# Kernel optimization log

Measured on AMD Instinct MI355X. Metric: run time of the kernel, lower is better.

Reference implementation:

```python
import jax, jax.numpy as jnp
import numpy as np

N_NODES = 50000
N_EDGES = 400000


def _gcn_norm(edge_index, num_nodes):
    """Add self-loops and compute symmetric GCN normalization coefficients.

    Returns (src, dst, norm) where out[dst] += norm * h[src].
    """
    loop = jnp.arange(num_nodes, dtype=edge_index.dtype)
    src = jnp.concatenate([edge_index[0], loop])
    dst = jnp.concatenate([edge_index[1], loop])
    ones = jnp.ones(src.shape[0], dtype=jnp.float32)
    deg = jax.ops.segment_sum(ones, dst, num_segments=num_nodes)
    d_inv_sqrt = jnp.where(deg > 0, jax.lax.rsqrt(jnp.maximum(deg, 1.0)), 0.0)
    norm = d_inv_sqrt[src] * d_inv_sqrt[dst]
    return src, dst, norm


def _gcn_conv(x, W, b, src, dst, norm, num_nodes):
    h = x @ W                              # [N, out] dense GEMM first (PyG GCNConv order)
    msg = h[src] * norm[:, None]           # [E+N, out] gather + scale
    agg = jax.ops.segment_sum(msg, dst, num_segments=num_nodes)  # scatter-add
    return agg + b


def setup_inputs() -> dict:
    key = jax.random.key(0)
    k1, k2, k3, k4, k5, k6 = jax.random.split(key, 6)
    x = jax.random.normal(k1, (N_NODES, 128), dtype=jnp.float32)
    edge_index = jax.random.randint(k2, (2, N_EDGES), 0, N_NODES, dtype=jnp.int64)
    # Glorot-ish scaled params
    W1 = jax.random.normal(k3, (128, 512), dtype=jnp.float32) * (1.0 / np.sqrt(128))
    b1 = jnp.zeros((512,), dtype=jnp.float32)
    W2 = jax.random.normal(k4, (512, 250), dtype=jnp.float32) * (1.0 / np.sqrt(512))
    b2 = jnp.zeros((250,), dtype=jnp.float32)
    return {"x": x, "edge_index": edge_index, "W1": W1, "b1": b1, "W2": W2, "b2": b2}


def reference(x, edge_index, W1, b1, W2, b2):
    num_nodes = x.shape[0]
    src, dst, norm = _gcn_norm(edge_index, num_nodes)
    h = _gcn_conv(x, W1, b1, src, dst, norm, num_nodes)
    h = jax.nn.relu(h)
    h = _gcn_conv(h, W2, b2, src, dst, norm, num_nodes)
    return jax.nn.relu(h)
```

## Files before the change

kernel.cpp:

```cpp
#include <hip/hip_runtime.h>

constexpr int NN  = 50000;
constexpr int NE  = 400000;
constexpr int F0  = 128;
constexpr int F1  = 512;
constexpr int F2  = 250;
constexpr int MT64 = 782;
constexpr int SLOT = 64;

typedef short  short8 __attribute__((ext_vector_type(8)));
typedef float  f32x4  __attribute__((ext_vector_type(4)));

__device__ inline unsigned short f2bf(float f) {
    union { float f; unsigned u; } v; v.f = f;
    unsigned u = v.u;
    return (unsigned short)((u + 0x7FFFu + ((u >> 16) & 1u)) >> 16);
}
__device__ inline float bf2f(unsigned short h) {
    union { unsigned u; float f; } v; v.u = ((unsigned)h) << 16;
    return v.f;
}
__device__ inline float bflo(unsigned u) {
    union { unsigned u; float f; } v; v.u = u << 16; return v.f;
}
__device__ inline float bfhi(unsigned u) {
    union { unsigned u; float f; } v; v.u = u & 0xFFFF0000u; return v.f;
}

__global__ void k_build(const int4* __restrict__ src4, const int4* __restrict__ dst4,
                        int* __restrict__ cnt, int* __restrict__ slot) {
    int t = blockIdx.x * 256 + threadIdx.x;
    if (t >= NE / 4) return;
    int4 s = src4[t];
    int4 d = dst4[t];
    int p;
    p = atomicAdd(&cnt[d.x], 1); if (p < SLOT) slot[d.x * SLOT + p] = s.x;
    p = atomicAdd(&cnt[d.y], 1); if (p < SLOT) slot[d.y * SLOT + p] = s.y;
    p = atomicAdd(&cnt[d.z], 1); if (p < SLOT) slot[d.z * SLOT + p] = s.z;
    p = atomicAdd(&cnt[d.w], 1); if (p < SLOT) slot[d.w * SLOT + p] = s.w;
}

__global__ __launch_bounds__(256) void k_prep(
        const float4* __restrict__ x4, const int* __restrict__ cnt,
        ushort4* __restrict__ xs,
        const float* __restrict__ W1, unsigned short* __restrict__ w1t,
        const float* __restrict__ W2, unsigned short* __restrict__ w2t) {
    int b = blockIdx.x;
    if (b < 6250) {
        int t = b * 256 + threadIdx.x;
        float dn = rsqrtf((float)cnt[t >> 5] + 1.0f);
        float4 v = x4[t];
        ushort4 o;
        o.x = f2bf(dn * v.x); o.y = f2bf(dn * v.y);
        o.z = f2bf(dn * v.z); o.w = f2bf(dn * v.w);
        xs[t] = o;
    } else if (b < 6250 + 256) {
        int t = (b - 6250) * 256 + threadIdx.x;
        int n = t >> 7, k = t & 127;
        w1t[t] = f2bf(W1[k * F1 + n]);
    } else {
        int t = (b - 6506) * 256 + threadIdx.x;
        int n = t >> 9, k = t & 511;
        w2t[t] = (n < F2) ? f2bf(W2[k * F2 + n]) : (unsigned short)0;
    }
}

__global__ __launch_bounds__(256) void k_gather1(
        const unsigned int* __restrict__ xs, const int* __restrict__ slot,
        const int* __restrict__ cnt, unsigned int* __restrict__ agg) {
    int n = blockIdx.x * 4 + (threadIdx.x >> 6);
    int c = threadIdx.x & 63;
    if (n >= NN) return;
    int deg = cnt[n]; if (deg > SLOT) deg = SLOT;
    float dn = rsqrtf((float)deg + 1.0f);
    const int* sl = slot + n * SLOT;
    unsigned a = xs[(size_t)n * 64 + c];
    float s0 = bflo(a), s1 = bfhi(a);
    int j = 0;
    for (; j + 8 <= deg; j += 8) {
        int i0 = sl[j],     i1 = sl[j + 1], i2 = sl[j + 2], i3 = sl[j + 3];
        int i4 = sl[j + 4], i5 = sl[j + 5], i6 = sl[j + 6], i7 = sl[j + 7];
        unsigned v0 = xs[(size_t)i0 * 64 + c];
        unsigned v1 = xs[(size_t)i1 * 64 + c];
        unsigned v2 = xs[(size_t)i2 * 64 + c];
        unsigned v3 = xs[(size_t)i3 * 64 + c];
        unsigned v4 = xs[(size_t)i4 * 64 + c];
        unsigned v5 = xs[(size_t)i5 * 64 + c];
        unsigned v6 = xs[(size_t)i6 * 64 + c];
        unsigned v7 = xs[(size_t)i7 * 64 + c];
        s0 += bflo(v0) + bflo(v1) + bflo(v2) + bflo(v3)
            + bflo(v4) + bflo(v5) + bflo(v6) + bflo(v7);
        s1 += bfhi(v0) + bfhi(v1) + bfhi(v2) + bfhi(v3)
            + bfhi(v4) + bfhi(v5) + bfhi(v6) + bfhi(v7);
    }
    for (; j + 4 <= deg; j += 4) {
        int i0 = sl[j], i1 = sl[j + 1], i2 = sl[j + 2], i3 = sl[j + 3];
        unsigned v0 = xs[(size_t)i0 * 64 + c];
        unsigned v1 = xs[(size_t)i1 * 64 + c];
        unsigned v2 = xs[(size_t)i2 * 64 + c];
        unsigned v3 = xs[(size_t)i3 * 64 + c];
        s0 += bflo(v0) + bflo(v1) + bflo(v2) + bflo(v3);
        s1 += bfhi(v0) + bfhi(v1) + bfhi(v2) + bfhi(v3);
    }
    for (; j < deg; ++j) {
        unsigned v = xs[(size_t)sl[j] * 64 + c];
        s0 += bflo(v); s1 += bfhi(v);
    }
    agg[(size_t)n * 64 + c] =
        (unsigned)f2bf(dn * s0) | ((unsigned)f2bf(dn * s1) << 16);
}

__global__ __launch_bounds__(256) void k_gemm1(
        const unsigned short* __restrict__ A,
        const unsigned short* __restrict__ Bt,
        unsigned short* __restrict__ C,
        const float* __restrict__ bias, int M)
{
    __shared__ unsigned short As[64 * 128];
    __shared__ unsigned short Bs[128 * 128];

    const int tid = threadIdx.x;
    const int wv = tid >> 6, ln = tid & 63;
    const int m0 = blockIdx.y * 64, n0 = blockIdx.x * 128;
    const int wy = wv >> 1, wx = wv & 1;
    const int lane15 = ln & 15, quad = ln >> 4;

#pragma unroll
    for (int i = 0; i < 4; ++i) {
        int c = i * 256 + tid;
        int m = c >> 4, q = c & 15;
        int gq = q ^ (m & 15);
        int arow = m0 + m; if (arow > M - 1) arow = M - 1;
        __builtin_amdgcn_global_load_lds(
            (const __attribute__((address_space(1))) void*)(A + (size_t)arow * 128 + gq * 8),
            (__attribute__((address_space(3))) void*)(As + (i * 4 + wv) * 512), 16, 0, 0);
    }
#pragma unroll
    for (int i = 0; i < 8; ++i) {
        int c = i * 256 + tid;
        int n = c >> 4, q = c & 15;
        int gq = q ^ (n & 15);
        __builtin_amdgcn_global_load_lds(
            (const __attribute__((address_space(1))) void*)(Bt + (size_t)(n0 + n) * 128 + gq * 8),
            (__attribute__((address_space(3))) void*)(Bs + (i * 4 + wv) * 512), 16, 0, 0);
    }

    f32x4 acc[2][4];
#pragma unroll
    for (int fy = 0; fy < 2; ++fy)
#pragma unroll
        for (int fx = 0; fx < 4; ++fx)
            acc[fy][fx] = (f32x4)0.0f;

    __syncthreads();

#pragma unroll
    for (int kk = 0; kk < 4; ++kk) {
        short8 af[2], bf[4];
#pragma unroll
        for (int f = 0; f < 2; ++f) {
            int mA = wy * 32 + f * 16 + lane15;
            int sA = (kk * 4 + quad) ^ (mA & 15);
            af[f] = *(const short8*)(As + mA * 128 + sA * 8);
        }
#pragma unroll
        for (int f = 0; f < 4; ++f) {
            int nB = wx * 64 + f * 16 + lane15;
            int sB = (kk * 4 + quad) ^ (nB & 15);
            bf[f] = *(const short8*)(Bs + nB * 128 + sB * 8);
        }
#pragma unroll
        for (int fy = 0; fy < 2; ++fy)
#pragma unroll
            for (int fx = 0; fx < 4; ++fx)
                acc[fy][fx] = __builtin_amdgcn_mfma_f32_16x16x32_bf16(
                    af[fy], bf[fx], acc[fy][fx], 0, 0, 0);
    }

#pragma unroll
    for (int fy = 0; fy < 2; ++fy) {
        int rowb = m0 + wy * 32 + fy * 16 + quad * 4;
#pragma unroll
        for (int fx = 0; fx < 4; ++fx) {
            int col = n0 + wx * 64 + fx * 16 + lane15;
            float bia = bias[col];
            f32x4 v = acc[fy][fx];
#pragma unroll
            for (int r = 0; r < 4; ++r) {
                int row = rowb + r;
                if (row < M)
                    C[(size_t)row * F1 + col] = f2bf(fmaxf(v[r] + bia, 0.0f));
            }
        }
    }
}

__global__ __launch_bounds__(256) void k_gemm2(
        const unsigned short* __restrict__ A,
        const unsigned short* __restrict__ Bt,
        unsigned short* __restrict__ C,
        const int* __restrict__ cnt, int M)
{
    __shared__ unsigned short As[2][64 * 32];
    __shared__ unsigned short Bs[2][256 * 32];

    const int tid = threadIdx.x;
    const int wv = tid >> 6, ln = tid & 63;
    const int m0 = blockIdx.x * 64;
    const int wy = wv >> 1, wx = wv & 1;
    const int lane15 = ln & 15, quad = ln >> 4;

    const int mA_ = tid >> 2, qA = tid & 3;
    const int gqA = qA ^ ((mA_ >> 1) & 3);
    int arow = m0 + mA_; if (arow > M - 1) arow = M - 1;
    const unsigned short* agp = A + (size_t)arow * F1 + gqA * 8;
    const int aofs = wv * 512;

    const unsigned short* bgp[4];
    int bofs[4];
#pragma unroll
    for (int i = 0; i < 4; ++i) {
        int c = (i * 4 + wv) * 64 + ln;
        int n = c >> 2, q = c & 3;
        int gq = q ^ ((n >> 1) & 3);
        bgp[i] = Bt + (size_t)n * F1 + gq * 8;
        bofs[i] = (i * 4 + wv) * 512;
    }

    f32x4 acc[2][8];
#pragma unroll
    for (int fy = 0; fy < 2; ++fy)
#pragma unroll
        for (int fx = 0; fx < 8; ++fx)
            acc[fy][fx] = (f32x4)0.0f;

    const int NK = F1 / 32;

    __builtin_amdgcn_global_load_lds(
        (const __attribute__((address_space(1))) void*)agp,
        (__attribute__((address_space(3))) void*)(&As[0][0] + aofs), 16, 0, 0);
#pragma unroll
    for (int i = 0; i < 4; ++i)
        __builtin_amdgcn_global_load_lds(
            (const __attribute__((address_space(1))) void*)bgp[i],
            (__attribute__((address_space(3))) void*)(&Bs[0][0] + bofs[i]), 16, 0, 0);

    for (int ks = 0; ks < NK; ++ks) {
        __syncthreads();
        if (ks + 1 < NK) {
            int ko = (ks + 1) << 5;
            int nb = (ks + 1) & 1;
            __builtin_amdgcn_global_load_lds(
                (const __attribute__((address_space(1))) void*)(agp + ko),
                (__attribute__((address_space(3))) void*)(&As[nb][0] + aofs), 16, 0, 0);
#pragma unroll
            for (int i = 0; i < 4; ++i)
                __builtin_amdgcn_global_load_lds(
                    (const __attribute__((address_space(1))) void*)(bgp[i] + ko),
                    (__attribute__((address_space(3))) void*)(&Bs[nb][0] + bofs[i]), 16, 0, 0);
        }
        const int b = ks & 1;
        short8 af[2], bf[8];
#pragma unroll
        for (int f = 0; f < 2; ++f) {
            int mA = wy * 32 + f * 16 + lane15;
            int sA = quad ^ ((mA >> 1) & 3);
            af[f] = *(const short8*)(&As[b][0] + mA * 32 + sA * 8);
        }
#pragma unroll
        for (int f = 0; f < 8; ++f) {
            int nB = wx * 128 + f * 16 + lane15;
            int sB = quad ^ ((nB >> 1) & 3);
            bf[f] = *(const short8*)(&Bs[b][0] + nB * 32 + sB * 8);
        }
#pragma unroll
        for (int fy = 0; fy < 2; ++fy)
#pragma unroll
            for (int fx = 0; fx < 8; ++fx)
                acc[fy][fx] = __builtin_amdgcn_mfma_f32_16x16x32_bf16(
                    af[fy], bf[fx], acc[fy][fx], 0, 0, 0);
    }

#pragma unroll
    for (int fy = 0; fy < 2; ++fy) {
        int rowb = m0 + wy * 32 + fy * 16 + quad * 4;
        float rs[4];
#pragma unroll
        for (int r = 0; r < 4; ++r) {
            int row = rowb + r; if (row > M - 1) row = M - 1;
            rs[r] = rsqrtf((float)cnt[row] + 1.0f);
        }
#pragma unroll
        for (int fx = 0; fx < 8; ++fx) {
            int col = wx * 128 + fx * 16 + lane15;
            f32x4 v = acc[fy][fx];
#pragma unroll
            for (int r = 0; r < 4; ++r) {
                int row = rowb + r;
                if (row < M)
                    C[(size_t)row * 256 + col] = f2bf(v[r] * rs[r]);
            }
        }
    }
}

__global__ __launch_bounds__(256) void k_gather2(
        const ushort4* __restrict__ t4, const int* __restrict__ slot,
        const int* __restrict__ cnt, const float* __restrict__ b2,
        float* __restrict__ out) {
    int n = blockIdx.x * 4 + (threadIdx.x >> 6);
    int c = threadIdx.x & 63;
    if (n >= NN) return;
    int deg = cnt[n]; if (deg > SLOT) deg = SLOT;
    float dn = rsqrtf((float)deg + 1.0f);
    const int* sl = slot + n * SLOT;
    ushort4 a = t4[(size_t)n * 64 + c];
    float sx = bf2f(a.x), sy = bf2f(a.y), sz = bf2f(a.z), sw = bf2f(a.w);
    int j = 0;
    for (; j + 8 <= deg; j += 8) {
        int i0 = sl[j],     i1 = sl[j + 1], i2 = sl[j + 2], i3 = sl[j + 3];
        int i4 = sl[j + 4], i5 = sl[j + 5], i6 = sl[j + 6], i7 = sl[j + 7];
        ushort4 v0 = t4[(size_t)i0 * 64 + c];
        ushort4 v1 = t4[(size_t)i1 * 64 + c];
        ushort4 v2 = t4[(size_t)i2 * 64 + c];
        ushort4 v3 = t4[(size_t)i3 * 64 + c];
        ushort4 v4 = t4[(size_t)i4 * 64 + c];
        ushort4 v5 = t4[(size_t)i5 * 64 + c];
        ushort4 v6 = t4[(size_t)i6 * 64 + c];
        ushort4 v7 = t4[(size_t)i7 * 64 + c];
        sx += bf2f(v0.x) + bf2f(v1.x) + bf2f(v2.x) + bf2f(v3.x)
            + bf2f(v4.x) + bf2f(v5.x) + bf2f(v6.x) + bf2f(v7.x);
        sy += bf2f(v0.y) + bf2f(v1.y) + bf2f(v2.y) + bf2f(v3.y)
            + bf2f(v4.y) + bf2f(v5.y) + bf2f(v6.y) + bf2f(v7.y);
        sz += bf2f(v0.z) + bf2f(v1.z) + bf2f(v2.z) + bf2f(v3.z)
            + bf2f(v4.z) + bf2f(v5.z) + bf2f(v6.z) + bf2f(v7.z);
        sw += bf2f(v0.w) + bf2f(v1.w) + bf2f(v2.w) + bf2f(v3.w)
            + bf2f(v4.w) + bf2f(v5.w) + bf2f(v6.w) + bf2f(v7.w);
    }
    for (; j + 4 <= deg; j += 4) {
        int i0 = sl[j], i1 = sl[j + 1], i2 = sl[j + 2], i3 = sl[j + 3];
        ushort4 v0 = t4[(size_t)i0 * 64 + c];
        ushort4 v1 = t4[(size_t)i1 * 64 + c];
        ushort4 v2 = t4[(size_t)i2 * 64 + c];
        ushort4 v3 = t4[(size_t)i3 * 64 + c];
        sx += bf2f(v0.x) + bf2f(v1.x) + bf2f(v2.x) + bf2f(v3.x);
        sy += bf2f(v0.y) + bf2f(v1.y) + bf2f(v2.y) + bf2f(v3.y);
        sz += bf2f(v0.z) + bf2f(v1.z) + bf2f(v2.z) + bf2f(v3.z);
        sw += bf2f(v0.w) + bf2f(v1.w) + bf2f(v2.w) + bf2f(v3.w);
    }
    for (; j < deg; ++j) {
        ushort4 v = t4[(size_t)sl[j] * 64 + c];
        sx += bf2f(v.x); sy += bf2f(v.y); sz += bf2f(v.z); sw += bf2f(v.w);
    }
    int f = c * 4;
    float* o = out + (size_t)n * F2;
    if (f     < F2) o[f]     = fmaxf(dn * sx + b2[f],     0.f);
    if (f + 1 < F2) o[f + 1] = fmaxf(dn * sy + b2[f + 1], 0.f);
    if (f + 2 < F2) o[f + 2] = fmaxf(dn * sz + b2[f + 2], 0.f);
    if (f + 3 < F2) o[f + 3] = fmaxf(dn * sw + b2[f + 3], 0.f);
}

extern "C" void kernel_launch(void* const* d_in, const int* in_sizes, int n_in,
                              void* d_out, int out_size, void* d_ws, size_t ws_size,
                              hipStream_t stream) {
    const float* x  = (const float*)d_in[0];
    const int*   ei = (const int*)d_in[1];
    const float* W1 = (const float*)d_in[2];
    const float* b1 = (const float*)d_in[3];
    const float* W2 = (const float*)d_in[4];
    const float* b2 = (const float*)d_in[5];
    float* out = (float*)d_out;

    char* p = (char*)d_ws;
    auto carve = [&](size_t bytes) { char* r = p; p += (bytes + 255) & ~(size_t)255; return r; };
    int*            cnt  = (int*)carve(NN * 4);
    int*            slot = (int*)carve((size_t)NN * SLOT * 4);
    unsigned short* xs   = (unsigned short*)carve((size_t)NN * F0 * 2);
    unsigned short* agg1 = (unsigned short*)carve((size_t)NN * F0 * 2);
    unsigned short* h1   = (unsigned short*)carve((size_t)NN * F1 * 2);
    unsigned short* t2s  = (unsigned short*)carve((size_t)NN * 256 * 2);
    unsigned short* w1t  = (unsigned short*)carve((size_t)F1 * F0 * 2);
    unsigned short* w2t  = (unsigned short*)carve((size_t)256 * F1 * 2);

    hipMemsetAsync(cnt, 0, NN * sizeof(int), stream);
    k_build<<<(NE / 4 + 255) / 256, 256, 0, stream>>>(
        (const int4*)ei, (const int4*)(ei + NE), cnt, slot);
    k_prep<<<6250 + 256 + 512, 256, 0, stream>>>(
        (const float4*)x, cnt, (ushort4*)xs, W1, w1t, W2, w2t);
    k_gather1<<<(NN + 3) / 4, 256, 0, stream>>>((const unsigned int*)xs, slot, cnt,
                                                (unsigned int*)agg1);
    k_gemm1<<<dim3(F1 / 128, MT64), 256, 0, stream>>>(agg1, w1t, h1, b1, NN);
    k_gemm2<<<MT64, 256, 0, stream>>>(h1, w2t, t2s, cnt, NN);
    k_gather2<<<(NN + 3) / 4, 256, 0, stream>>>((const ushort4*)t2s, slot, cnt, b2, out);
}
```

Before: 238.7 us.

## Fuse both GEMMs via shared-memory hidden tile and merge graph build with prep

Fuses the first GEMM (with bias and ReLU) and the second GEMM into one kernel. A 32-row tile of the hidden activations stays in shared memory instead of making a 50000x512 bf16 round trip through global memory. The graph build and input conversion kernels are merged into one launch. Because the count array is no longer finished when x is converted, the source-degree scaling moves into gather1, which costs a per-neighbour count load and rsqrt. The fused GEMM reloads all of W1 and W2 for every 32-row tile, and its wider shared-memory footprint may reduce occupancy.

```diff
diff --git a/kernel.cpp b/kernel.cpp
--- a/kernel.cpp
+++ b/kernel.cpp
@@ -5,7 +5,7 @@
 constexpr int F0  = 128;
 constexpr int F1  = 512;
 constexpr int F2  = 250;
-constexpr int MT64 = 782;
+constexpr int MT32 = 1564;
 constexpr int SLOT = 64;
 
 typedef short  short8 __attribute__((ext_vector_type(8)));
@@ -27,39 +27,39 @@
     union { unsigned u; float f; } v; v.u = u & 0xFFFF0000u; return v.f;
 }
 
-__global__ void k_build(const int4* __restrict__ src4, const int4* __restrict__ dst4,
-                        int* __restrict__ cnt, int* __restrict__ slot) {
-    int t = blockIdx.x * 256 + threadIdx.x;
-    if (t >= NE / 4) return;
-    int4 s = src4[t];
-    int4 d = dst4[t];
-    int p;
-    p = atomicAdd(&cnt[d.x], 1); if (p < SLOT) slot[d.x * SLOT + p] = s.x;
-    p = atomicAdd(&cnt[d.y], 1); if (p < SLOT) slot[d.y * SLOT + p] = s.y;
-    p = atomicAdd(&cnt[d.z], 1); if (p < SLOT) slot[d.z * SLOT + p] = s.z;
-    p = atomicAdd(&cnt[d.w], 1); if (p < SLOT) slot[d.w * SLOT + p] = s.w;
-}
-
-__global__ __launch_bounds__(256) void k_prep(
-        const float4* __restrict__ x4, const int* __restrict__ cnt,
-        ushort4* __restrict__ xs,
+#define GLDS(src, dst) __builtin_amdgcn_global_load_lds( \
+    (const __attribute__((address_space(1))) void*)(src), \
+    (__attribute__((address_space(3))) void*)(dst), 16, 0, 0)
+
+__global__ __launch_bounds__(256) void k_setup(
+        const int4* __restrict__ src4, const int4* __restrict__ dst4,
+        int* __restrict__ cnt, int* __restrict__ slot,
+        const float4* __restrict__ x4, ushort4* __restrict__ xs,
         const float* __restrict__ W1, unsigned short* __restrict__ w1t,
         const float* __restrict__ W2, unsigned short* __restrict__ w2t) {
     int b = blockIdx.x;
-    if (b < 6250) {
+    if (b < 391) {
         int t = b * 256 + threadIdx.x;
-        float dn = rsqrtf((float)cnt[t >> 5] + 1.0f);
+        if (t >= NE / 4) return;
+        int4 s = src4[t];
+        int4 d = dst4[t];
+        int p;
+        p = atomicAdd(&cnt[d.x], 1); if (p < SLOT) slot[d.x * SLOT + p] = s.x;
+        p = atomicAdd(&cnt[d.y], 1); if (p < SLOT) slot[d.y * SLOT + p] = s.y;
+        p = atomicAdd(&cnt[d.z], 1); if (p < SLOT) slot[d.z * SLOT + p] = s.z;
+        p = atomicAdd(&cnt[d.w], 1); if (p < SLOT) slot[d.w * SLOT + p] = s.w;
+    } else if (b < 391 + 6250) {
+        int t = (b - 391) * 256 + threadIdx.x;
         float4 v = x4[t];
         ushort4 o;
-        o.x = f2bf(dn * v.x); o.y = f2bf(dn * v.y);
-        o.z = f2bf(dn * v.z); o.w = f2bf(dn * v.w);
+        o.x = f2bf(v.x); o.y = f2bf(v.y); o.z = f2bf(v.z); o.w = f2bf(v.w);
         xs[t] = o;
-    } else if (b < 6250 + 256) {
-        int t = (b - 6250) * 256 + threadIdx.x;
+    } else if (b < 391 + 6250 + 256) {
+        int t = (b - 6641) * 256 + threadIdx.x;
         int n = t >> 7, k = t & 127;
         w1t[t] = f2bf(W1[k * F1 + n]);
     } else {
-        int t = (b - 6506) * 256 + threadIdx.x;
+        int t = (b - 6897) * 256 + threadIdx.x;
         int n = t >> 9, k = t & 511;
         w2t[t] = (n < F2) ? f2bf(W2[k * F2 + n]) : (unsigned short)0;
     }
@@ -71,15 +71,24 @@
     int n = blockIdx.x * 4 + (threadIdx.x >> 6);
     int c = threadIdx.x & 63;
     if (n >= NN) return;
-    int deg = cnt[n]; if (deg > SLOT) deg = SLOT;
+    int deg = cnt[n];
     float dn = rsqrtf((float)deg + 1.0f);
+    if (deg > SLOT) deg = SLOT;
     const int* sl = slot + n * SLOT;
     unsigned a = xs[(size_t)n * 64 + c];
-    float s0 = bflo(a), s1 = bfhi(a);
+    float s0 = dn * bflo(a), s1 = dn * bfhi(a);
     int j = 0;
     for (; j + 8 <= deg; j += 8) {
         int i0 = sl[j],     i1 = sl[j + 1], i2 = sl[j + 2], i3 = sl[j + 3];
         int i4 = sl[j + 4], i5 = sl[j + 5], i6 = sl[j + 6], i7 = sl[j + 7];
+        float w0 = rsqrtf((float)cnt[i0] + 1.0f);
+        float w1 = rsqrtf((float)cnt[i1] + 1.0f);
+        float w2 = rsqrtf((float)cnt[i2] + 1.0f);
+        float w3 = rsqrtf((float)cnt[i3] + 1.0f);
+        float w4 = rsqrtf((float)cnt[i4] + 1.0f);
+        float w5 = rsqrtf((float)cnt[i5] + 1.0f);
+        float w6 = rsqrtf((float)cnt[i6] + 1.0f);
+        float w7 = rsqrtf((float)cnt[i7] + 1.0f);
         unsigned v0 = xs[(size_t)i0 * 64 + c];
         unsigned v1 = xs[(size_t)i1 * 64 + c];
         unsigned v2 = xs[(size_t)i2 * 64 + c];
@@ -88,218 +97,140 @@
         unsigned v5 = xs[(size_t)i5 * 64 + c];
         unsigned v6 = xs[(size_t)i6 * 64 + c];
         unsigned v7 = xs[(size_t)i7 * 64 + c];
-        s0 += bflo(v0) + bflo(v1) + bflo(v2) + bflo(v3)
-            + bflo(v4) + bflo(v5) + bflo(v6) + bflo(v7);
-        s1 += bfhi(v0) + bfhi(v1) + bfhi(v2) + bfhi(v3)
-            + bfhi(v4) + bfhi(v5) + bfhi(v6) + bfhi(v7);
-    }
-    for (; j + 4 <= deg; j += 4) {
-        int i0 = sl[j], i1 = sl[j + 1], i2 = sl[j + 2], i3 = sl[j + 3];
-        unsigned v0 = xs[(size_t)i0 * 64 + c];
-        unsigned v1 = xs[(size_t)i1 * 64 + c];
-        unsigned v2 = xs[(size_t)i2 * 64 + c];
-        unsigned v3 = xs[(size_t)i3 * 64 + c];
-        s0 += bflo(v0) + bflo(v1) + bflo(v2) + bflo(v3);
-        s1 += bfhi(v0) + bfhi(v1) + bfhi(v2) + bfhi(v3);
+        s0 += w0 * bflo(v0) + w1 * bflo(v1) + w2 * bflo(v2) + w3 * bflo(v3)
+            + w4 * bflo(v4) + w5 * bflo(v5) + w6 * bflo(v6) + w7 * bflo(v7);
+        s1 += w0 * bfhi(v0) + w1 * bfhi(v1) + w2 * bfhi(v2) + w3 * bfhi(v3)
+            + w4 * bfhi(v4) + w5 * bfhi(v5) + w6 * bfhi(v6) + w7 * bfhi(v7);
     }
     for (; j < deg; ++j) {
-        unsigned v = xs[(size_t)sl[j] * 64 + c];
-        s0 += bflo(v); s1 += bfhi(v);
+        int s = sl[j];
+        float w = rsqrtf((float)cnt[s] + 1.0f);
+        unsigned v = xs[(size_t)s * 64 + c];
+        s0 += w * bflo(v); s1 += w * bfhi(v);
     }
     agg[(size_t)n * 64 + c] =
         (unsigned)f2bf(dn * s0) | ((unsigned)f2bf(dn * s1) << 16);
 }
 
-__global__ __launch_bounds__(256) void k_gemm1(
+__global__ __launch_bounds__(256, 2) void k_gemm12(
         const unsigned short* __restrict__ A,
-        const unsigned short* __restrict__ Bt,
-        unsigned short* __restrict__ C,
-        const float* __restrict__ bias, int M)
+        const unsigned short* __restrict__ W1t,
+        const unsigned short* __restrict__ W2t,
+        const float* __restrict__ b1,
+        const int* __restrict__ cnt,
+        unsigned short* __restrict__ C)
 {
-    __shared__ unsigned short As[64 * 128];
-    __shared__ unsigned short Bs[128 * 128];
+    __shared__ __align__(16) unsigned short smem[32768];
+    unsigned short* As  = smem;
+    unsigned short* Bs1 = smem + 4096;
+    unsigned short* H   = smem + 16384;
+    unsigned short* B2a = smem;
+    unsigned short* B2b = smem + 8192;
 
     const int tid = threadIdx.x;
     const int wv = tid >> 6, ln = tid & 63;
-    const int m0 = blockIdx.y * 64, n0 = blockIdx.x * 128;
-    const int wy = wv >> 1, wx = wv & 1;
+    const int m0 = blockIdx.x * 32;
+    const int wy = wv & 1, wx = wv >> 1;
     const int lane15 = ln & 15, quad = ln >> 4;
+
+    float b1v[16];
+#pragma unroll
+    for (int nb = 0; nb < 8; ++nb)
+#pragma unroll
+        for (int fx = 0; fx < 2; ++fx)
+            b1v[nb * 2 + fx] = b1[nb * 64 + wx * 32 + fx * 16 + lane15];
+
+#pragma unroll
+    for (int i = 0; i < 2; ++i) {
+        int c = i * 256 + tid;
+        int m = c >> 4, q = c & 15, gq = q ^ (m & 15);
+        int ar = m0 + m; if (ar > NN - 1) ar = NN - 1;
+        GLDS(A + (size_t)ar * 128 + gq * 8, As + (i * 4 + wv) * 512);
+    }
+
+    for (int nb = 0; nb < 8; ++nb) {
+#pragma unroll
+        for (int i = 0; i < 4; ++i) {
+            int c = i * 256 + tid;
+            int rr = c >> 4, q = c & 15, gq = q ^ (rr & 15);
+            GLDS(W1t + (size_t)(nb * 64 + rr) * 128 + gq * 8, Bs1 + (i * 4 + wv) * 512);
+        }
+        __syncthreads();
+
+        f32x4 acc1[2] = {(f32x4)0.0f, (f32x4)0.0f};
+#pragma unroll
+        for (int ks = 0; ks < 4; ++ks) {
+            int mA = wy * 16 + lane15;
+            short8 af = *(const short8*)(As + mA * 128 + (((ks * 4 + quad) ^ lane15) << 3));
+#pragma unroll
+            for (int fx = 0; fx < 2; ++fx) {
+                int rr = wx * 32 + fx * 16 + lane15;
+                short8 bf = *(const short8*)(Bs1 + rr * 128 + (((ks * 4 + quad) ^ (rr & 15)) << 3));
+                acc1[fx] = __builtin_amdgcn_mfma_f32_16x16x32_bf16(af, bf, acc1[fx], 0, 0, 0);
+            }
+        }
+#pragma unroll
+        for (int fx = 0; fx < 2; ++fx) {
+            int cc = nb * 64 + wx * 32 + fx * 16 + lane15;
+            float bia = b1v[nb * 2 + fx];
+#pragma unroll
+            for (int r = 0; r < 4; ++r) {
+                int rr = wy * 16 + quad * 4 + r;
+                float val = fmaxf(acc1[fx][r] + bia, 0.0f);
+                H[rr * 512 + (((cc >> 3) ^ (rr & 15)) << 3) + (cc & 7)] = f2bf(val);
+            }
+        }
+        __syncthreads();
+    }
+
+    f32x4 acc[8];
+#pragma unroll
+    for (int fx = 0; fx < 8; ++fx) acc[fx] = (f32x4)0.0f;
 
 #pragma unroll
     for (int i = 0; i < 4; ++i) {
         int c = i * 256 + tid;
-        int m = c >> 4, q = c & 15;
-        int gq = q ^ (m & 15);
-        int arow = m0 + m; if (arow > M - 1) arow = M - 1;
-        __builtin_amdgcn_global_load_lds(
-            (const __attribute__((address_space(1))) void*)(A + (size_t)arow * 128 + gq * 8),
-            (__attribute__((address_space(3))) void*)(As + (i * 4 + wv) * 512), 16, 0, 0);
-    }
-#pragma unroll
-    for (int i = 0; i < 8; ++i) {
-        int c = i * 256 + tid;
-        int n = c >> 4, q = c & 15;
-        int gq = q ^ (n & 15);
-        __builtin_amdgcn_global_load_lds(
-            (const __attribute__((address_space(1))) void*)(Bt + (size_t)(n0 + n) * 128 + gq * 8),
-            (__attribute__((address_space(3))) void*)(Bs + (i * 4 + wv) * 512), 16, 0, 0);
-    }
-
-    f32x4 acc[2][4];
-#pragma unroll
-    for (int fy = 0; fy < 2; ++fy)
-#pragma unroll
-        for (int fx = 0; fx < 4; ++fx)
-            acc[fy][fx] = (f32x4)0.0f;
-
-    __syncthreads();
-
-#pragma unroll
-    for (int kk = 0; kk < 4; ++kk) {
-        short8 af[2], bf[4];
-#pragma unroll
-        for (int f = 0; f < 2; ++f) {
-            int mA = wy * 32 + f * 16 + lane15;
-            int sA = (kk * 4 + quad) ^ (mA & 15);
-            af[f] = *(const short8*)(As + mA * 128 + sA * 8);
-        }
-#pragma unroll
-        for (int f = 0; f < 4; ++f) {
-            int nB = wx * 64 + f * 16 + lane15;
-            int sB = (kk * 4 + quad) ^ (nB & 15);
-            bf[f] = *(const short8*)(Bs + nB * 128 + sB * 8);
-        }
-#pragma unroll
-        for (int fy = 0; fy < 2; ++fy)
-#pragma unroll
-            for (int fx = 0; fx < 4; ++fx)
-                acc[fy][fx] = __builtin_amdgcn_mfma_f32_16x16x32_bf16(
-                    af[fy], bf[fx], acc[fy][fx], 0, 0, 0);
-    }
-
-#pragma unroll
-    for (int fy = 0; fy < 2; ++fy) {
-        int rowb = m0 + wy * 32 + fy * 16 + quad * 4;
-#pragma unroll
-        for (int fx = 0; fx < 4; ++fx) {
-            int col = n0 + wx * 64 + fx * 16 + lane15;
-            float bia = bias[col];
-            f32x4 v = acc[fy][fx];
-#pragma unroll
-            for (int r = 0; r < 4; ++r) {
-                int row = rowb + r;
-                if (row < M)
-                    C[(size_t)row * F1 + col] = f2bf(fmaxf(v[r] + bia, 0.0f));
+        int n = c >> 2, q = c & 3, gq = q ^ ((n >> 1) & 3);
+        GLDS(W2t + (size_t)n * 512 + gq * 8, B2a + (i * 4 + wv) * 512);
+    }
+    for (int ks = 0; ks < 16; ++ks) {
+        __syncthreads();
+        if (ks + 1 < 16) {
+            unsigned short* nbuf = ((ks + 1) & 1) ? B2b : B2a;
+            int ko = (ks + 1) << 5;
+#pragma unroll
+            for (int i = 0; i < 4; ++i) {
+                int c = i * 256 + tid;
+                int n = c >> 2, q = c & 3, gq = q ^ ((n >> 1) & 3);
+                GLDS(W2t + (size_t)n * 512 + ko + gq * 8, nbuf + (i * 4 + wv) * 512);
             }
         }
-    }
-}
-
-__global__ __launch_bounds__(256) void k_gemm2(
-        const unsigned short* __restrict__ A,
-        const unsigned short* __restrict__ Bt,
-        unsigned short* __restrict__ C,
-        const int* __restrict__ cnt, int M)
-{
-    __shared__ unsigned short As[2][64 * 32];
-    __shared__ unsigned short Bs[2][256 * 32];
-
-    const int tid = threadIdx.x;
-    const int wv = tid >> 6, ln = tid & 63;
-    const int m0 = blockIdx.x * 64;
-    const int wy = wv >> 1, wx = wv & 1;
-    const int lane15 = ln & 15, quad = ln >> 4;
-
-    const int mA_ = tid >> 2, qA = tid & 3;
-    const int gqA = qA ^ ((mA_ >> 1) & 3);
-    int arow = m0 + mA_; if (arow > M - 1) arow = M - 1;
-    const unsigned short* agp = A + (size_t)arow * F1 + gqA * 8;
-    const int aofs = wv * 512;
-
-    const unsigned short* bgp[4];
-    int bofs[4];
-#pragma unroll
-    for (int i = 0; i < 4; ++i) {
-        int c = (i * 4 + wv) * 64 + ln;
-        int n = c >> 2, q = c & 3;
-        int gq = q ^ ((n >> 1) & 3);
-        bgp[i] = Bt + (size_t)n * F1 + gq * 8;
-        bofs[i] = (i * 4 + wv) * 512;
-    }
-
-    f32x4 acc[2][8];
-#pragma unroll
-    for (int fy = 0; fy < 2; ++fy)
-#pragma unroll
-        for (int fx = 0; fx < 8; ++fx)
-            acc[fy][fx] = (f32x4)0.0f;
-
-    const int NK = F1 / 32;
-
-    __builtin_amdgcn_global_load_lds(
-        (const __attribute__((address_space(1))) void*)agp,
-        (__attribute__((address_space(3))) void*)(&As[0][0] + aofs), 16, 0, 0);
-#pragma unroll
-    for (int i = 0; i < 4; ++i)
-        __builtin_amdgcn_global_load_lds(
-            (const __attribute__((address_space(1))) void*)bgp[i],
-            (__attribute__((address_space(3))) void*)(&Bs[0][0] + bofs[i]), 16, 0, 0);
-
-    for (int ks = 0; ks < NK; ++ks) {
-        __syncthreads();
-        if (ks + 1 < NK) {
-            int ko = (ks + 1) << 5;
-            int nb = (ks + 1) & 1;
-            __builtin_amdgcn_global_load_lds(
-                (const __attribute__((address_space(1))) void*)(agp + ko),
-                (__attribute__((address_space(3))) void*)(&As[nb][0] + aofs), 16, 0, 0);
-#pragma unroll
-            for (int i = 0; i < 4; ++i)
-                __builtin_amdgcn_global_load_lds(
-                    (const __attribute__((address_space(1))) void*)(bgp[i] + ko),
-                    (__attribute__((address_space(3))) void*)(&Bs[nb][0] + bofs[i]), 16, 0, 0);
-        }
-        const int b = ks & 1;
-        short8 af[2], bf[8];
-#pragma unroll
-        for (int f = 0; f < 2; ++f) {
-            int mA = wy * 32 + f * 16 + lane15;
-            int sA = quad ^ ((mA >> 1) & 3);
-            af[f] = *(const short8*)(&As[b][0] + mA * 32 + sA * 8);
-        }
-#pragma unroll
-        for (int f = 0; f < 8; ++f) {
-            int nB = wx * 128 + f * 16 + lane15;
-            int sB = quad ^ ((nB >> 1) & 3);
-            bf[f] = *(const short8*)(&Bs[b][0] + nB * 32 + sB * 8);
-        }
-#pragma unroll
-        for (int fy = 0; fy < 2; ++fy)
-#pragma unroll
-            for (int fx = 0; fx < 8; ++fx)
-                acc[fy][fx] = __builtin_amdgcn_mfma_f32_16x16x32_bf16(
-                    af[fy], bf[fx], acc[fy][fx], 0, 0, 0);
-    }
-
-#pragma unroll
-    for (int fy = 0; fy < 2; ++fy) {
-        int rowb = m0 + wy * 32 + fy * 16 + quad * 4;
-        float rs[4];
+        const unsigned short* bb = (ks & 1) ? B2b : B2a;
+        int mA = wy * 16 + lane15;
+        short8 af = *(const short8*)(H + mA * 512 + (((ks * 4 + quad) ^ lane15) << 3));
+#pragma unroll
+        for (int fx = 0; fx < 8; ++fx) {
+            int n = wx * 128 + fx * 16 + lane15;
+            short8 bf = *(const short8*)(bb + n * 32 + ((quad ^ ((n >> 1) & 3)) << 3));
+            acc[fx] = __builtin_amdgcn_mfma_f32_16x16x32_bf16(af, bf, acc[fx], 0, 0, 0);
+        }
+    }
+
+    int rowb = m0 + wy * 16 + quad * 4;
+    float rs[4];
+#pragma unroll
+    for (int r = 0; r < 4; ++r) {
+        int row = rowb + r; if (row > NN - 1) row = NN - 1;
+        rs[r] = rsqrtf((float)cnt[row] + 1.0f);
+    }
+#pragma unroll
+    for (int fx = 0; fx < 8; ++fx) {
+        int col = wx * 128 + fx * 16 + lane15;
 #pragma unroll
         for (int r = 0; r < 4; ++r) {
-            int row = rowb + r; if (row > M - 1) row = M - 1;
-            rs[r] = rsqrtf((float)cnt[row] + 1.0f);
-        }
-#pragma unroll
-        for (int fx = 0; fx < 8; ++fx) {
-            int col = wx * 128 + fx * 16 + lane15;
-            f32x4 v = acc[fy][fx];
-#pragma unroll
-            for (int r = 0; r < 4; ++r) {
-                int row = rowb + r;
-                if (row < M)
-                    C[(size_t)row * 256 + col] = f2bf(v[r] * rs[r]);
-            }
+            int row = rowb + r;
+            if (row < NN)
+                C[(size_t)row * 256 + col] = f2bf(acc[fx][r] * rs[r]);
         }
     }
 }
@@ -311,8 +242,9 @@
     int n = blockIdx.x * 4 + (threadIdx.x >> 6);
     int c = threadIdx.x & 63;
     if (n >= NN) return;
-    int deg = cnt[n]; if (deg > SLOT) deg = SLOT;
+    int deg = cnt[n];
     float dn = rsqrtf((float)deg + 1.0f);
+    if (deg > SLOT) deg = SLOT;
     const int* sl = slot + n * SLOT;
     ushort4 a = t4[(size_t)n * 64 + c];
     float sx = bf2f(a.x), sy = bf2f(a.y), sz = bf2f(a.z), sw = bf2f(a.w);
@@ -337,17 +269,6 @@
         sw += bf2f(v0.w) + bf2f(v1.w) + bf2f(v2.w) + bf2f(v3.w)
             + bf2f(v4.w) + bf2f(v5.w) + bf2f(v6.w) + bf2f(v7.w);
     }
-    for (; j + 4 <= deg; j += 4) {
-        int i0 = sl[j], i1 = sl[j + 1], i2 = sl[j + 2], i3 = sl[j + 3];
-        ushort4 v0 = t4[(size_t)i0 * 64 + c];
-        ushort4 v1 = t4[(size_t)i1 * 64 + c];
-        ushort4 v2 = t4[(size_t)i2 * 64 + c];
-        ushort4 v3 = t4[(size_t)i3 * 64 + c];
-        sx += bf2f(v0.x) + bf2f(v1.x) + bf2f(v2.x) + bf2f(v3.x);
-        sy += bf2f(v0.y) + bf2f(v1.y) + bf2f(v2.y) + bf2f(v3.y);
-        sz += bf2f(v0.z) + bf2f(v1.z) + bf2f(v2.z) + bf2f(v3.z);
-        sw += bf2f(v0.w) + bf2f(v1.w) + bf2f(v2.w) + bf2f(v3.w);
-    }
     for (; j < deg; ++j) {
         ushort4 v = t4[(size_t)sl[j] * 64 + c];
         sx += bf2f(v.x); sy += bf2f(v.y); sz += bf2f(v.z); sw += bf2f(v.w);
@@ -377,19 +298,16 @@
     int*            slot = (int*)carve((size_t)NN * SLOT * 4);
     unsigned short* xs   = (unsigned short*)carve((size_t)NN * F0 * 2);
     unsigned short* agg1 = (unsigned short*)carve((size_t)NN * F0 * 2);
-    unsigned short* h1   = (unsigned short*)carve((size_t)NN * F1 * 2);
     unsigned short* t2s  = (unsigned short*)carve((size_t)NN * 256 * 2);
     unsigned short* w1t  = (unsigned short*)carve((size_t)F1 * F0 * 2);
     unsigned short* w2t  = (unsigned short*)carve((size_t)256 * F1 * 2);
 
     hipMemsetAsync(cnt, 0, NN * sizeof(int), stream);
-    k_build<<<(NE / 4 + 255) / 256, 256, 0, stream>>>(
-        (const int4*)ei, (const int4*)(ei + NE), cnt, slot);
-    k_prep<<<6250 + 256 + 512, 256, 0, stream>>>(
-        (const float4*)x, cnt, (ushort4*)xs, W1, w1t, W2, w2t);
+    k_setup<<<391 + 6250 + 256 + 512, 256, 0, stream>>>(
+        (const int4*)ei, (const int4*)(ei + NE), cnt, slot,
+        (const float4*)x, (ushort4*)xs, W1, w1t, W2, w2t);
     k_gather1<<<(NN + 3) / 4, 256, 0, stream>>>((const unsigned int*)xs, slot, cnt,
                                                 (unsigned int*)agg1);
-    k_gemm1<<<dim3(F1 / 128, MT64), 256, 0, stream>>>(agg1, w1t, h1, b1, NN);
-    k_gemm2<<<MT64, 256, 0, stream>>>(h1, w2t, t2s, cnt, NN);
+    k_gemm12<<<MT32, 256, 0, stream>>>(agg1, w1t, w2t, b1, cnt, t2s);
     k_gather2<<<(NN + 3) / 4, 256, 0, stream>>>((const ushort4*)t2s, slot, cnt, b2, out);
 }
```

Result: no change. 239.3 us (+0.2%).
